# Performance work log

Measured on AMD Instinct MI355X. Metric: run time of the kernel, lower is better.

## Reference

```python
import jax, jax.numpy as jnp
import numpy as np

B, L, SH, EH, A, T = 128, 200, 512, 512, 512, 3


def setup_inputs() -> dict:
    key = jax.random.key(0)
    ks = jax.random.split(key, 13)
    s = 0.05  # small init scale to keep tanh/sigmoid unsaturated
    return {
        "sent_enc_doc": jax.random.normal(ks[0], (B, L, 2 * SH), jnp.float32),
        "h0_w": jax.random.normal(ks[1], (EH, SH), jnp.float32) * s,
        "h0_b": jax.random.normal(ks[2], (EH,), jnp.float32) * s,
        "gru_w_ih": jax.random.normal(ks[3], (3 * EH, 2 * SH), jnp.float32) * s,
        "gru_w_hh": jax.random.normal(ks[4], (3 * EH, EH), jnp.float32) * s,
        "gru_b_ih": jax.random.normal(ks[5], (3 * EH,), jnp.float32) * s,
        "gru_b_hh": jax.random.normal(ks[6], (3 * EH,), jnp.float32) * s,
        "wq": jax.random.normal(ks[7], (A, EH), jnp.float32) * s,
        "bq": jax.random.normal(ks[8], (A,), jnp.float32) * s,
        "wd": jax.random.normal(ks[9], (A, 2 * SH), jnp.float32) * s,
        "bd": jax.random.normal(ks[10], (A,), jnp.float32) * s,
        "ws": jax.random.normal(ks[11], (1, A), jnp.float32) * s,
        "bs": jax.random.normal(ks[12], (1,), jnp.float32) * s,
    }


def reference(sent_enc_doc, h0_w, h0_b, gru_w_ih, gru_w_hh, gru_b_ih, gru_b_hh,
              wq, bq, wd, bd, ws, bs):
    b, l, d2 = sent_enc_doc.shape
    sh = d2 // 2
    eh = gru_w_hh.shape[1]
    neg = jnp.asarray(-1e6, sent_enc_doc.dtype)

    # h0 = tanh(W * last backward vector), replicated across doc_len
    last_back = sent_enc_doc[:, 0, sh:]                      # (B, SH)
    h0 = jnp.tanh(last_back @ h0_w.T + h0_b)                 # (B, EH)
    h = jnp.broadcast_to(h0[:, None, :], (b, l, eh))         # (B, L, EH)

    s_prev = jnp.zeros((b, l, d2), sent_enc_doc.dtype)
    d_proj = sent_enc_doc @ wd.T + bd                        # (B, L, A) - loop-invariant
    mask = jnp.zeros((b, l), bool)
    rows = jnp.arange(b)

    scores_list, sel_list = [], []
    for _ in range(T):  # fixed, tiny, sequentially-dependent loop
        # GRUCell (torch gate order: r, z, n)
        gx = s_prev @ gru_w_ih.T + gru_b_ih                  # (B, L, 3EH)
        gh = h @ gru_w_hh.T + gru_b_hh                       # (B, L, 3EH)
        xr, xz, xn = jnp.split(gx, 3, axis=-1)
        hr, hz, hn = jnp.split(gh, 3, axis=-1)
        r = jax.nn.sigmoid(xr + hr)
        z = jax.nn.sigmoid(xz + hz)
        n = jnp.tanh(xn + r * hn)
        h = (1.0 - z) * n + z * h                            # (B, L, EH)

        # scorer: ws . tanh(Wq h + Wd s_i)
        score = (jnp.tanh(h @ wq.T + bq + d_proj) @ ws.T + bs)[..., 0]  # (B, L)
        score = jnp.where(mask, neg, score)
        idx = jnp.argmax(score, axis=1)                      # (B,)
        mask = mask.at[rows, idx].set(True)

        # gather the selected sentence encoding, broadcast to all positions
        s_sel = jnp.take_along_axis(sent_enc_doc, idx[:, None, None], axis=1)  # (B,1,2SH)
        s_prev = jnp.broadcast_to(s_sel, (b, l, d2))

        scores_list.append(score)
        sel_list.append(idx)

    sents_scores = jnp.stack(scores_list, axis=1)            # (B, T, L)
    sents_selected = jnp.stack(sel_list, axis=1)             # (B, T)
    return sents_scores, sents_selected
```

## Files before the change

kernel.cpp:

```cpp
#include <hip/hip_runtime.h>
#include <hip/hip_bf16.h>

constexpr int Bn  = 128;
constexpr int Ln  = 200;
constexpr int D2n = 1024;
constexpr int G3n = 1536;
constexpr int Tn  = 3;
constexpr int Nn  = 512;
constexpr int Kn  = 1024;

typedef unsigned short ushort;
typedef float f32x4 __attribute__((ext_vector_type(4)));
typedef __bf16 bf16x8 __attribute__((ext_vector_type(8)));

__device__ __forceinline__ ushort f2bf(float f) {
  unsigned u = __float_as_uint(f);
  unsigned r = (u + 0x7fffu + ((u >> 16) & 1u)) >> 16;
  return (ushort)r;
}
__device__ __forceinline__ float bf2f(ushort h) {
  return __uint_as_float(((unsigned)h) << 16);
}

__device__ __forceinline__ void gld_lds16(const ushort* g, ushort* l) {
  __builtin_amdgcn_global_load_lds(
      (const __attribute__((address_space(1))) unsigned int*)g,
      (__attribute__((address_space(3))) unsigned int*)l, 16, 0, 0);
}

__global__ void k_gather_lastb(const float* __restrict__ sent, float* __restrict__ lastb) {
  int i = blockIdx.x * 256 + threadIdx.x;
  int b = i >> 9, k = i & 511;
  lastb[i] = sent[(size_t)b * (Ln * D2n) + 512 + k];
}

__global__ void k_split(const float* __restrict__ W, ushort* __restrict__ hi,
                        ushort* __restrict__ lo) {
  int i = blockIdx.x * 256 + threadIdx.x;
  float4 v = ((const float4*)W)[i];
  ushort4 h, l;
  h.x = f2bf(v.x); l.x = f2bf(v.x - bf2f(h.x));
  h.y = f2bf(v.y); l.y = f2bf(v.y - bf2f(h.y));
  h.z = f2bf(v.z); l.z = f2bf(v.z - bf2f(h.z));
  h.w = f2bf(v.w); l.w = f2bf(v.w - bf2f(h.w));
  ((ushort4*)hi)[i] = h;
  ((ushort4*)lo)[i] = l;
}

template<int K, int ACT>
__launch_bounds__(256)
__global__ void k_small_gemm(const float* __restrict__ in, const float* __restrict__ W,
                             const float* __restrict__ bias, float* __restrict__ out, int J) {
  __shared__ float s[16 * K];
  const int b0 = blockIdx.y * 16;
  const int jl = threadIdx.x & 63;
  const int j  = blockIdx.x * 64 + jl;
  const int bg = (threadIdx.x >> 6) * 4;

  const float4* inp4 = (const float4*)(in + (size_t)b0 * K);
  float4* s4 = (float4*)s;
  for (int i = threadIdx.x; i < 4 * K; i += 256) s4[i] = inp4[i];
  __syncthreads();

  const float4* w4 = (const float4*)(W + (size_t)j * K);
  const float4* r0 = (const float4*)(s + (size_t)(bg + 0) * K);
  const float4* r1 = (const float4*)(s + (size_t)(bg + 1) * K);
  const float4* r2 = (const float4*)(s + (size_t)(bg + 2) * K);
  const float4* r3 = (const float4*)(s + (size_t)(bg + 3) * K);

  float acc0 = 0.f, acc1 = 0.f, acc2 = 0.f, acc3 = 0.f;
  #pragma unroll 4
  for (int k4 = 0; k4 < K / 4; ++k4) {
    float4 wv = w4[k4];
    float4 a;
    a = r0[k4]; acc0 += wv.x*a.x + wv.y*a.y + wv.z*a.z + wv.w*a.w;
    a = r1[k4]; acc1 += wv.x*a.x + wv.y*a.y + wv.z*a.z + wv.w*a.w;
    a = r2[k4]; acc2 += wv.x*a.x + wv.y*a.y + wv.z*a.z + wv.w*a.w;
    a = r3[k4]; acc3 += wv.x*a.x + wv.y*a.y + wv.z*a.z + wv.w*a.w;
  }
  float bb = bias[j];
  float v;
  v = acc0 + bb; if (ACT) v = tanhf(v); out[(size_t)(b0 + bg + 0) * J + j] = v;
  v = acc1 + bb; if (ACT) v = tanhf(v); out[(size_t)(b0 + bg + 1) * J + j] = v;
  v = acc2 + bb; if (ACT) v = tanhf(v); out[(size_t)(b0 + bg + 2) * J + j] = v;
  v = acc3 + bb; if (ACT) v = tanhf(v); out[(size_t)(b0 + bg + 3) * J + j] = v;
}

constexpr int NSTEP = Kn / 32;

__launch_bounds__(256)
__global__ void k_dproj_mfma(const ushort* __restrict__ Ahi, const ushort* __restrict__ Alo,
                             const ushort* __restrict__ Whi, const ushort* __restrict__ Wlo,
                             const float* __restrict__ bias, float* __restrict__ C) {
  __shared__ __align__(16) ushort sAh[128 * 32];
  __shared__ __align__(16) ushort sAl[128 * 32];
  __shared__ __align__(16) ushort sBh[128 * 32];
  __shared__ __align__(16) ushort sBl[128 * 32];

  const int bid = blockIdx.x;
  const int m0  = (bid % 200) * 128;
  const int n0  = (bid / 200) * 128;

  const int tid  = threadIdx.x;
  const int wave = tid >> 6, lane = tid & 63;
  const int wy = (wave >> 1) * 64, wx = (wave & 1) * 64;
  const int lm = lane & 15, lq = lane >> 4;

  const int fs = (lq ^ ((lm >> 1) & 3)) * 8;

  const int S0 = (wave * 2 + 0) * 64 + lane;
  const int S1 = (wave * 2 + 1) * 64 + lane;
  const int r0 = S0 >> 2, r1 = S1 >> 2;
  const int c0 = ((S0 & 3) ^ ((r0 >> 1) & 3)) * 8;
  const int c1 = ((S1 & 3) ^ ((r1 >> 1) & 3)) * 8;
  const ushort* pAh0 = Ahi + (size_t)(m0 + r0) * Kn + c0;
  const ushort* pAh1 = Ahi + (size_t)(m0 + r1) * Kn + c1;
  const ushort* pAl0 = Alo + (size_t)(m0 + r0) * Kn + c0;
  const ushort* pAl1 = Alo + (size_t)(m0 + r1) * Kn + c1;
  const ushort* pBh0 = Whi + (size_t)(n0 + r0) * Kn + c0;
  const ushort* pBh1 = Whi + (size_t)(n0 + r1) * Kn + c1;
  const ushort* pBl0 = Wlo + (size_t)(n0 + r0) * Kn + c0;
  const ushort* pBl1 = Wlo + (size_t)(n0 + r1) * Kn + c1;
  ushort* dA0 = &sAh[S0 * 8]; ushort* dA1 = &sAh[S1 * 8];
  ushort* dL0 = &sAl[S0 * 8]; ushort* dL1 = &sAl[S1 * 8];
  ushort* dB0 = &sBh[S0 * 8]; ushort* dB1 = &sBh[S1 * 8];
  ushort* dC0 = &sBl[S0 * 8]; ushort* dC1 = &sBl[S1 * 8];

  f32x4 acc[4][4] = {};

  for (int ks = 0; ks < NSTEP; ++ks) {
    const int ko = ks * 32;
    gld_lds16(pAh0 + ko, dA0); gld_lds16(pAh1 + ko, dA1);
    gld_lds16(pAl0 + ko, dL0); gld_lds16(pAl1 + ko, dL1);
    gld_lds16(pBh0 + ko, dB0); gld_lds16(pBh1 + ko, dB1);
    gld_lds16(pBl0 + ko, dC0); gld_lds16(pBl1 + ko, dC1);
    __syncthreads();

    bf16x8 ah[4], al[4], bh[4], bl[4];
    #pragma unroll
    for (int mi = 0; mi < 4; ++mi) {
      const int o = (wy + mi * 16 + lm) * 32 + fs;
      ah[mi] = *(const bf16x8*)&sAh[o];
      al[mi] = *(const bf16x8*)&sAl[o];
    }
    #pragma unroll
    for (int ni = 0; ni < 4; ++ni) {
      const int o = (wx + ni * 16 + lm) * 32 + fs;
      bh[ni] = *(const bf16x8*)&sBh[o];
      bl[ni] = *(const bf16x8*)&sBl[o];
    }
    #pragma unroll
    for (int mi = 0; mi < 4; ++mi)
      #pragma unroll
      for (int ni = 0; ni < 4; ++ni) {
        acc[mi][ni] = __builtin_amdgcn_mfma_f32_16x16x32_bf16(ah[mi], bh[ni], acc[mi][ni], 0, 0, 0);
        acc[mi][ni] = __builtin_amdgcn_mfma_f32_16x16x32_bf16(ah[mi], bl[ni], acc[mi][ni], 0, 0, 0);
        acc[mi][ni] = __builtin_amdgcn_mfma_f32_16x16x32_bf16(al[mi], bh[ni], acc[mi][ni], 0, 0, 0);
      }
    __syncthreads();
  }

  #pragma unroll
  for (int ni = 0; ni < 4; ++ni) {
    int col = n0 + wx + ni * 16 + lm;
    float bb = bias[col];
    #pragma unroll
    for (int mi = 0; mi < 4; ++mi) {
      int rbase = m0 + wy + mi * 16 + lq * 4;
      #pragma unroll
      for (int r = 0; r < 4; ++r)
        C[(size_t)(rbase + r) * Nn + col] = acc[mi][ni][r] + bb;
    }
  }
}

__global__ void k_gru_pw(const float* __restrict__ gx, const float* __restrict__ gh,
                         float* __restrict__ h) {
  int i = blockIdx.x * 256 + threadIdx.x;
  int b = i >> 9, j = i & 511;
  const float* gxb = gx + (size_t)b * G3n;
  const float* ghb = gh + (size_t)b * G3n;
  float rg = 1.f / (1.f + expf(-(gxb[j] + ghb[j])));
  float zg = 1.f / (1.f + expf(-(gxb[512 + j] + ghb[512 + j])));
  float ng = tanhf(gxb[1024 + j] + rg * ghb[1024 + j]);
  h[i] = (1.f - zg) * ng + zg * h[i];
}

__launch_bounds__(256)
__global__ void k_score(const float* __restrict__ dproj, const float* __restrict__ q,
                        const float* __restrict__ wsv, const float* __restrict__ bsv,
                        const int* __restrict__ mask, float* __restrict__ scoresf,
                        float* __restrict__ outScores, int t) {
  int w = blockIdx.x * 4 + (threadIdx.x >> 6);
  int lane = threadIdx.x & 63;
  int b = w / Ln, l = w % Ln;
  const float4* dp4 = (const float4*)(dproj + (size_t)w * Nn);
  const float4* q4  = (const float4*)(q + (size_t)b * Nn);
  const float4* ws4 = (const float4*)wsv;

  float sum = 0.f;
  #pragma unroll
  for (int i = 0; i < 2; ++i) {
    int idx = lane + i * 64;
    float4 d = dp4[idx], qq = q4[idx], wv = ws4[idx];
    sum += tanhf(qq.x + d.x) * wv.x + tanhf(qq.y + d.y) * wv.y
         + tanhf(qq.z + d.z) * wv.z + tanhf(qq.w + d.w) * wv.w;
  }
  #pragma unroll
  for (int off = 32; off > 0; off >>= 1) sum += __shfl_xor(sum, off, 64);

  if (lane == 0) {
    float v = sum + bsv[0];
    if (mask[w]) v = -1000000.0f;
    scoresf[w] = v;
    outScores[(size_t)b * (Tn * Ln) + t * Ln + l] = v;
  }
}

__launch_bounds__(256)
__global__ void k_argmax(const float* __restrict__ scoresf, const float* __restrict__ sent,
                         float* __restrict__ s_row, int* __restrict__ mask,
                         float* __restrict__ outSel, int t) {
  int b = blockIdx.x;
  __shared__ int s_idx;
  int tid = threadIdx.x;
  if (tid < 64) {
    const float* sc = scoresf + (size_t)b * Ln;
    float best = -3.0e38f; int bi = 0;
    for (int l = tid; l < Ln; l += 64) {
      float v = sc[l];
      if (v > best) { best = v; bi = l; }
    }
    #pragma unroll
    for (int off = 32; off > 0; off >>= 1) {
      float ov = __shfl_down(best, off, 64);
      int   oi = __shfl_down(bi,   off, 64);
      if (ov > best || (ov == best && oi < bi)) { best = ov; bi = oi; }
    }
    if (tid == 0) s_idx = bi;
  }
  __syncthreads();
  int idx = s_idx;
  const float* src = sent + ((size_t)b * Ln + idx) * D2n;
  float* dstp = s_row + (size_t)b * D2n;
  int k = tid * 4;
  *(float4*)(dstp + k) = *(const float4*)(src + k);
  if (tid == 0) {
    mask[b * Ln + idx] = 1;
    outSel[(size_t)b * Tn + t] = (float)idx;
  }
}

extern "C" void kernel_launch(void* const* d_in, const int* in_sizes, int n_in,
                              void* d_out, int out_size, void* d_ws, size_t ws_size,
                              hipStream_t stream) {
  const float* sent = (const float*)d_in[0];
  const float* h0_w = (const float*)d_in[1];
  const float* h0_b = (const float*)d_in[2];
  const float* w_ih = (const float*)d_in[3];
  const float* w_hh = (const float*)d_in[4];
  const float* b_ih = (const float*)d_in[5];
  const float* b_hh = (const float*)d_in[6];
  const float* wq   = (const float*)d_in[7];
  const float* bq   = (const float*)d_in[8];
  const float* wd   = (const float*)d_in[9];
  const float* bd   = (const float*)d_in[10];
  const float* wsv  = (const float*)d_in[11];
  const float* bsv  = (const float*)d_in[12];

  float* wsf     = (float*)d_ws;
  float* d_proj  = wsf;
  float* s_row   = d_proj + 13107200;
  float* h       = s_row + 131072;
  float* gx      = h + 65536;
  float* gh      = gx + 196608;
  float* lastb   = gh + 196608;
  float* q       = lastb + 65536;
  float* scoresf = q + 65536;
  int*   mask    = (int*)(scoresf + 25600);
  ushort* Whi    = (ushort*)(mask + 25600);
  ushort* Wlo    = Whi + 524288;
  ushort* Ahi    = Wlo + 524288;
  ushort* Alo    = Ahi + 26214400;

  float* outScores = (float*)d_out;
  float* outSel    = outScores + (size_t)Bn * Tn * Ln;

  hipMemsetAsync(s_row, 0, 131072 * sizeof(float), stream);
  hipMemsetAsync(mask, 0, 25600 * sizeof(int), stream);

  k_gather_lastb<<<256, 256, 0, stream>>>(sent, lastb);
  k_small_gemm<512, 1><<<dim3(8, 8), 256, 0, stream>>>(lastb, h0_w, h0_b, h, 512);
  k_split<<<512, 256, 0, stream>>>(wd, Whi, Wlo);
  k_split<<<25600, 256, 0, stream>>>(sent, Ahi, Alo);
  k_dproj_mfma<<<800, 256, 0, stream>>>(Ahi, Alo, Whi, Wlo, bd, d_proj);

  for (int t = 0; t < Tn; ++t) {
    k_small_gemm<1024, 0><<<dim3(24, 8), 256, 0, stream>>>(s_row, w_ih, b_ih, gx, G3n);
    k_small_gemm<512, 0><<<dim3(24, 8), 256, 0, stream>>>(h, w_hh, b_hh, gh, G3n);
    k_gru_pw<<<256, 256, 0, stream>>>(gx, gh, h);
    k_small_gemm<512, 0><<<dim3(8, 8), 256, 0, stream>>>(h, wq, bq, q, 512);
    k_score<<<6400, 256, 0, stream>>>(d_proj, q, wsv, bsv, mask, scoresf, outScores, t);
    k_argmax<<<128, 256, 0, stream>>>(scoresf, sent, s_row, mask, outSel, t);
  }
}
```

Measured before the change: 619.3 us.

## Fuse GRU gate GEMMs with pointwise update, transpose weights, atomic-packed argmax

The two gate GEMMs and the GRU pointwise kernel are replaced by one fused kernel that reads pre-transposed W_ih/W_hh with coalesced column access and splits K across two wave halves. The query projection likewise uses a transposed Wq. Argmax now happens inside the score kernel through a 64-bit atomicMax on a packed (ordered float, inverted index) key, so the argmax kernel only decodes the key. This removes per-step launches and intermediate gx/gh traffic, at the cost of three transposes per call and per-row atomic contention.

```diff
diff --git a/kernel.cpp b/kernel.cpp
--- a/kernel.cpp
+++ b/kernel.cpp
@@ -26,6 +26,12 @@
   __builtin_amdgcn_global_load_lds(
       (const __attribute__((address_space(1))) unsigned int*)g,
       (__attribute__((address_space(3))) unsigned int*)l, 16, 0, 0);
+}
+
+__device__ __forceinline__ unsigned long long score_key(float v, int l) {
+  unsigned u = __float_as_uint(v);
+  unsigned k32 = (u & 0x80000000u) ? ~u : (u | 0x80000000u);
+  return ((unsigned long long)k32 << 32) | (unsigned)(~l);
 }
 
 __global__ void k_gather_lastb(const float* __restrict__ sent, float* __restrict__ lastb) {
@@ -45,6 +51,20 @@
   h.w = f2bf(v.w); l.w = f2bf(v.w - bf2f(h.w));
   ((ushort4*)hi)[i] = h;
   ((ushort4*)lo)[i] = l;
+}
+
+__global__ void k_transp(const float* __restrict__ in, float* __restrict__ out,
+                         int R, int C) {
+  __shared__ float t[32][33];
+  const int x = threadIdx.x, y = threadIdx.y;
+  const int c0 = blockIdx.x * 32, r0 = blockIdx.y * 32;
+  #pragma unroll
+  for (int i = 0; i < 4; ++i)
+    t[y + i * 8][x] = in[(size_t)(r0 + y + i * 8) * C + c0 + x];
+  __syncthreads();
+  #pragma unroll
+  for (int i = 0; i < 4; ++i)
+    out[(size_t)(c0 + y + i * 8) * R + r0 + x] = t[x][y + i * 8];
 }
 
 template<int K, int ACT>
@@ -174,22 +194,110 @@
   }
 }
 
-__global__ void k_gru_pw(const float* __restrict__ gx, const float* __restrict__ gh,
-                         float* __restrict__ h) {
-  int i = blockIdx.x * 256 + threadIdx.x;
-  int b = i >> 9, j = i & 511;
-  const float* gxb = gx + (size_t)b * G3n;
-  const float* ghb = gh + (size_t)b * G3n;
-  float rg = 1.f / (1.f + expf(-(gxb[j] + ghb[j])));
-  float zg = 1.f / (1.f + expf(-(gxb[512 + j] + ghb[512 + j])));
-  float ng = tanhf(gxb[1024 + j] + rg * ghb[1024 + j]);
-  h[i] = (1.f - zg) * ng + zg * h[i];
+__launch_bounds__(512)
+__global__ void k_gru(const float* __restrict__ s_row, const float* __restrict__ h_old,
+                      const float* __restrict__ wihT, const float* __restrict__ whhT,
+                      const float* __restrict__ b_ih, const float* __restrict__ b_hh,
+                      float* __restrict__ h_new) {
+  __shared__ __align__(16) float sS[4][1024];
+  __shared__ __align__(16) float sH[4][512];
+  __shared__ float sP[256][6];
+
+  const int tid  = threadIdx.x;
+  const int lane = tid & 63;
+  const int wave = tid >> 6;
+  const int b_loc = wave & 3, kh = wave >> 2;
+  const int jt = blockIdx.x & 7, bt = blockIdx.x >> 3;
+  const int j  = jt * 64 + lane;
+
+  {
+    const float4* src = (const float4*)(s_row + (size_t)bt * 4 * 1024);
+    float4* dst = (float4*)&sS[0][0];
+    dst[tid] = src[tid];
+    dst[tid + 512] = src[tid + 512];
+    ((float4*)&sH[0][0])[tid] = ((const float4*)(h_old + (size_t)bt * 4 * 512))[tid];
+  }
+  __syncthreads();
+
+  float xr = 0, xz = 0, xn = 0, hr = 0, hz = 0, hn = 0;
+  {
+    const float* w = wihT + (size_t)(kh * 512) * G3n + j;
+    const float4* sv4 = (const float4*)&sS[b_loc][kh * 512];
+    #pragma unroll 2
+    for (int k4 = 0; k4 < 128; ++k4) {
+      float4 sv = sv4[k4];
+      xr += w[0] * sv.x; xz += w[512] * sv.x; xn += w[1024] * sv.x; w += G3n;
+      xr += w[0] * sv.y; xz += w[512] * sv.y; xn += w[1024] * sv.y; w += G3n;
+      xr += w[0] * sv.z; xz += w[512] * sv.z; xn += w[1024] * sv.z; w += G3n;
+      xr += w[0] * sv.w; xz += w[512] * sv.w; xn += w[1024] * sv.w; w += G3n;
+    }
+  }
+  {
+    const float* w = whhT + (size_t)(kh * 256) * G3n + j;
+    const float4* hv4 = (const float4*)&sH[b_loc][kh * 256];
+    #pragma unroll 2
+    for (int k4 = 0; k4 < 64; ++k4) {
+      float4 hv = hv4[k4];
+      hr += w[0] * hv.x; hz += w[512] * hv.x; hn += w[1024] * hv.x; w += G3n;
+      hr += w[0] * hv.y; hz += w[512] * hv.y; hn += w[1024] * hv.y; w += G3n;
+      hr += w[0] * hv.z; hz += w[512] * hv.z; hn += w[1024] * hv.z; w += G3n;
+      hr += w[0] * hv.w; hz += w[512] * hv.w; hn += w[1024] * hv.w; w += G3n;
+    }
+  }
+  const int pidx = b_loc * 64 + lane;
+  if (kh) {
+    sP[pidx][0] = xr; sP[pidx][1] = xz; sP[pidx][2] = xn;
+    sP[pidx][3] = hr; sP[pidx][4] = hz; sP[pidx][5] = hn;
+  }
+  __syncthreads();
+  if (!kh) {
+    xr += sP[pidx][0]; xz += sP[pidx][1]; xn += sP[pidx][2];
+    hr += sP[pidx][3]; hz += sP[pidx][4]; hn += sP[pidx][5];
+    xr += b_ih[j];        hr += b_hh[j];
+    xz += b_ih[512 + j];  hz += b_hh[512 + j];
+    xn += b_ih[1024 + j]; hn += b_hh[1024 + j];
+    float r = 1.f / (1.f + expf(-(xr + hr)));
+    float z = 1.f / (1.f + expf(-(xz + hz)));
+    float n = tanhf(xn + r * hn);
+    const int b = bt * 4 + b_loc;
+    float hold = sH[b_loc][j];
+    h_new[(size_t)b * 512 + j] = (1.f - z) * n + z * hold;
+  }
+}
+
+__launch_bounds__(256)
+__global__ void k_qT(const float* __restrict__ h, const float* __restrict__ wqT,
+                     const float* __restrict__ bq, float* __restrict__ q) {
+  __shared__ __align__(16) float sH[4][512];
+  const int tid = threadIdx.x, lane = tid & 63, bw = tid >> 6;
+  const int jt = blockIdx.x & 7, bt = blockIdx.x >> 3;
+  const int j = jt * 64 + lane;
+  {
+    float4* dst = (float4*)&sH[0][0];
+    const float4* src = (const float4*)(h + (size_t)bt * 2048);
+    dst[tid] = src[tid];
+    dst[tid + 256] = src[tid + 256];
+  }
+  __syncthreads();
+  float acc = 0.f;
+  const float* w = wqT + j;
+  const float4* hv4 = (const float4*)&sH[bw][0];
+  #pragma unroll 4
+  for (int k4 = 0; k4 < 128; ++k4) {
+    float4 hv = hv4[k4];
+    acc += w[0] * hv.x; w += 512;
+    acc += w[0] * hv.y; w += 512;
+    acc += w[0] * hv.z; w += 512;
+    acc += w[0] * hv.w; w += 512;
+  }
+  const int b = bt * 4 + bw;
+  q[(size_t)b * 512 + j] = acc + bq[j];
 }
 
 __launch_bounds__(256)
 __global__ void k_score(const float* __restrict__ dproj, const float* __restrict__ q,
                         const float* __restrict__ wsv, const float* __restrict__ bsv,
-                        const int* __restrict__ mask, float* __restrict__ scoresf,
+                        const int* __restrict__ mask, unsigned long long* __restrict__ packed,
                         float* __restrict__ outScores, int t) {
   int w = blockIdx.x * 4 + (threadIdx.x >> 6);
   int lane = threadIdx.x & 63;
@@ -212,32 +320,22 @@
   if (lane == 0) {
     float v = sum + bsv[0];
     if (mask[w]) v = -1000000.0f;
-    scoresf[w] = v;
     outScores[(size_t)b * (Tn * Ln) + t * Ln + l] = v;
+    atomicMax(&packed[b], score_key(v, l));
   }
 }
 
 __launch_bounds__(256)
-__global__ void k_argmax(const float* __restrict__ scoresf, const float* __restrict__ sent,
+__global__ void k_argmax(unsigned long long* __restrict__ packed,
+                         const float* __restrict__ sent,
                          float* __restrict__ s_row, int* __restrict__ mask,
                          float* __restrict__ outSel, int t) {
   int b = blockIdx.x;
   __shared__ int s_idx;
   int tid = threadIdx.x;
-  if (tid < 64) {
-    const float* sc = scoresf + (size_t)b * Ln;
-    float best = -3.0e38f; int bi = 0;
-    for (int l = tid; l < Ln; l += 64) {
-      float v = sc[l];
-      if (v > best) { best = v; bi = l; }
-    }
-    #pragma unroll
-    for (int off = 32; off > 0; off >>= 1) {
-      float ov = __shfl_down(best, off, 64);
-      int   oi = __shfl_down(bi,   off, 64);
-      if (ov > best || (ov == best && oi < bi)) { best = ov; bi = oi; }
-    }
-    if (tid == 0) s_idx = bi;
+  if (tid == 0) {
+    unsigned long long key = packed[b];
+    s_idx = (int)(~(unsigned)(key & 0xFFFFFFFFull));
   }
   __syncthreads();
   int idx = s_idx;
@@ -248,6 +346,7 @@
   if (tid == 0) {
     mask[b * Ln + idx] = 1;
     outSel[(size_t)b * Tn + t] = (float)idx;
+    packed[b] = 0ull;
   }
 }
 
@@ -271,14 +370,16 @@
   float* wsf     = (float*)d_ws;
   float* d_proj  = wsf;
   float* s_row   = d_proj + 13107200;
-  float* h       = s_row + 131072;
-  float* gx      = h + 65536;
-  float* gh      = gx + 196608;
-  float* lastb   = gh + 196608;
+  float* hA      = s_row + 131072;
+  float* hB      = hA + 65536;
+  float* lastb   = hB + 65536;
   float* q       = lastb + 65536;
-  float* scoresf = q + 65536;
-  int*   mask    = (int*)(scoresf + 25600);
-  ushort* Whi    = (ushort*)(mask + 25600);
+  float* wihT    = q + 65536;
+  float* whhT    = wihT + 1572864;
+  float* wqT     = whhT + 786432;
+  int*   mask    = (int*)(wqT + 262144);
+  unsigned long long* packed = (unsigned long long*)(mask + 25600);
+  ushort* Whi    = (ushort*)(packed + 128);
   ushort* Wlo    = Whi + 524288;
   ushort* Ahi    = Wlo + 524288;
   ushort* Alo    = Ahi + 26214400;
@@ -288,19 +389,24 @@
 
   hipMemsetAsync(s_row, 0, 131072 * sizeof(float), stream);
   hipMemsetAsync(mask, 0, 25600 * sizeof(int), stream);
+  hipMemsetAsync(packed, 0, 128 * sizeof(unsigned long long), stream);
 
   k_gather_lastb<<<256, 256, 0, stream>>>(sent, lastb);
-  k_small_gemm<512, 1><<<dim3(8, 8), 256, 0, stream>>>(lastb, h0_w, h0_b, h, 512);
+  k_small_gemm<512, 1><<<dim3(8, 8), 256, 0, stream>>>(lastb, h0_w, h0_b, hA, 512);
+  k_transp<<<dim3(32, 48), dim3(32, 8), 0, stream>>>(w_ih, wihT, 1536, 1024);
+  k_transp<<<dim3(16, 48), dim3(32, 8), 0, stream>>>(w_hh, whhT, 1536, 512);
+  k_transp<<<dim3(16, 16), dim3(32, 8), 0, stream>>>(wq, wqT, 512, 512);
   k_split<<<512, 256, 0, stream>>>(wd, Whi, Wlo);
   k_split<<<25600, 256, 0, stream>>>(sent, Ahi, Alo);
   k_dproj_mfma<<<800, 256, 0, stream>>>(Ahi, Alo, Whi, Wlo, bd, d_proj);
 
+  float* hc = hA;
+  float* hn = hB;
   for (int t = 0; t < Tn; ++t) {
-    k_small_gemm<1024, 0><<<dim3(24, 8), 256, 0, stream>>>(s_row, w_ih, b_ih, gx, G3n);
-    k_small_gemm<512, 0><<<dim3(24, 8), 256, 0, stream>>>(h, w_hh, b_hh, gh, G3n);
-    k_gru_pw<<<256, 256, 0, stream>>>(gx, gh, h);
-    k_small_gemm<512, 0><<<dim3(8, 8), 256, 0, stream>>>(h, wq, bq, q, 512);
-    k_score<<<6400, 256, 0, stream>>>(d_proj, q, wsv, bsv, mask, scoresf, outScores, t);
-    k_argmax<<<128, 256, 0, stream>>>(scoresf, sent, s_row, mask, outSel, t);
-  }
-}
+    k_gru<<<256, 512, 0, stream>>>(s_row, hc, wihT, whhT, b_ih, b_hh, hn);
+    k_qT<<<256, 256, 0, stream>>>(hn, wqT, bq, q);
+    k_score<<<6400, 256, 0, stream>>>(d_proj, q, wsv, bsv, mask, packed, outScores, t);
+    k_argmax<<<128, 256, 0, stream>>>(packed, sent, s_row, mask, outSel, t);
+    float* tmp = hc; hc = hn; hn = tmp;
+  }
+}
```

Result: slower. 752.9 us (+21.6%).

## Fuse the per-step GRU/score/argmax loop into one cooperative persistent kernel

Applied to the files above, without the earlier changes.

Replaces the 18 per-timestep kernel launches with a single cooperative kernel of 256 blocks that loops over the three steps and separates stages with grid-wide syncs. The gx and gh GEMMs now run in the same phase instead of two launches. This removes launch overhead and inter-kernel gaps. The cost is grid.sync overhead, lower parallelism for the score stage (256 blocks looping over 6400 work items), and a 64KB shared buffer per block that limits occupancy.

```diff
diff --git a/kernel.cpp b/kernel.cpp
--- a/kernel.cpp
+++ b/kernel.cpp
@@ -1,5 +1,8 @@
 #include <hip/hip_runtime.h>
 #include <hip/hip_bf16.h>
+#include <hip/hip_cooperative_groups.h>
+
+namespace cg = cooperative_groups;
 
 constexpr int Bn  = 128;
 constexpr int Ln  = 200;
@@ -48,18 +51,20 @@
 }
 
 template<int K, int ACT>
-__launch_bounds__(256)
-__global__ void k_small_gemm(const float* __restrict__ in, const float* __restrict__ W,
-                             const float* __restrict__ bias, float* __restrict__ out, int J) {
-  __shared__ float s[16 * K];
-  const int b0 = blockIdx.y * 16;
-  const int jl = threadIdx.x & 63;
-  const int j  = blockIdx.x * 64 + jl;
-  const int bg = (threadIdx.x >> 6) * 4;
+__device__ __forceinline__ void gemm_work(const float* __restrict__ in,
+                                          const float* __restrict__ W,
+                                          const float* __restrict__ bias,
+                                          float* __restrict__ out, int J,
+                                          int jt, int bt, float* s) {
+  const int tid = threadIdx.x;
+  const int b0 = bt * 16;
+  const int jl = tid & 63;
+  const int j  = jt * 64 + jl;
+  const int bg = (tid >> 6) * 4;
 
   const float4* inp4 = (const float4*)(in + (size_t)b0 * K);
   float4* s4 = (float4*)s;
-  for (int i = threadIdx.x; i < 4 * K; i += 256) s4[i] = inp4[i];
+  for (int i = tid; i < 4 * K; i += 256) s4[i] = inp4[i];
   __syncthreads();
 
   const float4* w4 = (const float4*)(W + (size_t)j * K);
@@ -84,6 +89,15 @@
   v = acc1 + bb; if (ACT) v = tanhf(v); out[(size_t)(b0 + bg + 1) * J + j] = v;
   v = acc2 + bb; if (ACT) v = tanhf(v); out[(size_t)(b0 + bg + 2) * J + j] = v;
   v = acc3 + bb; if (ACT) v = tanhf(v); out[(size_t)(b0 + bg + 3) * J + j] = v;
+  __syncthreads();
+}
+
+template<int K, int ACT>
+__launch_bounds__(256)
+__global__ void k_small_gemm(const float* __restrict__ in, const float* __restrict__ W,
+                             const float* __restrict__ bias, float* __restrict__ out, int J) {
+  __shared__ float s[16 * K];
+  gemm_work<K, ACT>(in, W, bias, out, J, blockIdx.x, blockIdx.y, s);
 }
 
 constexpr int NSTEP = Kn / 32;
@@ -174,80 +188,105 @@
   }
 }
 
-__global__ void k_gru_pw(const float* __restrict__ gx, const float* __restrict__ gh,
-                         float* __restrict__ h) {
-  int i = blockIdx.x * 256 + threadIdx.x;
-  int b = i >> 9, j = i & 511;
-  const float* gxb = gx + (size_t)b * G3n;
-  const float* ghb = gh + (size_t)b * G3n;
-  float rg = 1.f / (1.f + expf(-(gxb[j] + ghb[j])));
-  float zg = 1.f / (1.f + expf(-(gxb[512 + j] + ghb[512 + j])));
-  float ng = tanhf(gxb[1024 + j] + rg * ghb[1024 + j]);
-  h[i] = (1.f - zg) * ng + zg * h[i];
-}
-
 __launch_bounds__(256)
-__global__ void k_score(const float* __restrict__ dproj, const float* __restrict__ q,
+__global__ void k_tloop(const float* __restrict__ sent,
+                        const float* __restrict__ w_ih, const float* __restrict__ w_hh,
+                        const float* __restrict__ b_ih, const float* __restrict__ b_hh,
+                        const float* __restrict__ wq, const float* __restrict__ bq,
                         const float* __restrict__ wsv, const float* __restrict__ bsv,
-                        const int* __restrict__ mask, float* __restrict__ scoresf,
-                        float* __restrict__ outScores, int t) {
-  int w = blockIdx.x * 4 + (threadIdx.x >> 6);
-  int lane = threadIdx.x & 63;
-  int b = w / Ln, l = w % Ln;
-  const float4* dp4 = (const float4*)(dproj + (size_t)w * Nn);
-  const float4* q4  = (const float4*)(q + (size_t)b * Nn);
-  const float4* ws4 = (const float4*)wsv;
-
-  float sum = 0.f;
-  #pragma unroll
-  for (int i = 0; i < 2; ++i) {
-    int idx = lane + i * 64;
-    float4 d = dp4[idx], qq = q4[idx], wv = ws4[idx];
-    sum += tanhf(qq.x + d.x) * wv.x + tanhf(qq.y + d.y) * wv.y
-         + tanhf(qq.z + d.z) * wv.z + tanhf(qq.w + d.w) * wv.w;
-  }
-  #pragma unroll
-  for (int off = 32; off > 0; off >>= 1) sum += __shfl_xor(sum, off, 64);
-
-  if (lane == 0) {
-    float v = sum + bsv[0];
-    if (mask[w]) v = -1000000.0f;
-    scoresf[w] = v;
-    outScores[(size_t)b * (Tn * Ln) + t * Ln + l] = v;
-  }
-}
-
-__launch_bounds__(256)
-__global__ void k_argmax(const float* __restrict__ scoresf, const float* __restrict__ sent,
-                         float* __restrict__ s_row, int* __restrict__ mask,
-                         float* __restrict__ outSel, int t) {
-  int b = blockIdx.x;
+                        const float* __restrict__ dproj,
+                        float* __restrict__ s_row, float* __restrict__ h,
+                        float* __restrict__ gx, float* __restrict__ gh,
+                        float* __restrict__ q, float* __restrict__ scoresf,
+                        int* __restrict__ mask,
+                        float* __restrict__ outScores, float* __restrict__ outSel) {
+  cg::grid_group grid = cg::this_grid();
+  __shared__ float sbuf[16 * 1024];
   __shared__ int s_idx;
-  int tid = threadIdx.x;
-  if (tid < 64) {
-    const float* sc = scoresf + (size_t)b * Ln;
-    float best = -3.0e38f; int bi = 0;
-    for (int l = tid; l < Ln; l += 64) {
-      float v = sc[l];
-      if (v > best) { best = v; bi = l; }
-    }
-    #pragma unroll
-    for (int off = 32; off > 0; off >>= 1) {
-      float ov = __shfl_down(best, off, 64);
-      int   oi = __shfl_down(bi,   off, 64);
-      if (ov > best || (ov == best && oi < bi)) { best = ov; bi = oi; }
-    }
-    if (tid == 0) s_idx = bi;
-  }
-  __syncthreads();
-  int idx = s_idx;
-  const float* src = sent + ((size_t)b * Ln + idx) * D2n;
-  float* dstp = s_row + (size_t)b * D2n;
-  int k = tid * 4;
-  *(float4*)(dstp + k) = *(const float4*)(src + k);
-  if (tid == 0) {
-    mask[b * Ln + idx] = 1;
-    outSel[(size_t)b * Tn + t] = (float)idx;
+
+  const int bid = blockIdx.x;
+  const int tid = threadIdx.x;
+
+  for (int t = 0; t < Tn; ++t) {
+    for (int w = bid; w < 384; w += 256) {
+      if (w < 192) gemm_work<1024, 0>(s_row, w_ih, b_ih, gx, G3n, w % 24, w / 24, sbuf);
+      else { int v = w - 192; gemm_work<512, 0>(h, w_hh, b_hh, gh, G3n, v % 24, v / 24, sbuf); }
+    }
+    grid.sync();
+
+    {
+      int i = bid * 256 + tid;
+      int b = i >> 9, j = i & 511;
+      const float* gxb = gx + (size_t)b * G3n;
+      const float* ghb = gh + (size_t)b * G3n;
+      float rg = 1.f / (1.f + expf(-(gxb[j] + ghb[j])));
+      float zg = 1.f / (1.f + expf(-(gxb[512 + j] + ghb[512 + j])));
+      float ng = tanhf(gxb[1024 + j] + rg * ghb[1024 + j]);
+      h[i] = (1.f - zg) * ng + zg * h[i];
+    }
+    grid.sync();
+
+    for (int w = bid; w < 64; w += 256)
+      gemm_work<512, 0>(h, wq, bq, q, 512, w % 8, w / 8, sbuf);
+    grid.sync();
+
+    for (int blk = bid; blk < 6400; blk += 256) {
+      int w = blk * 4 + (tid >> 6);
+      int lane = tid & 63;
+      int b = w / Ln, l = w % Ln;
+      const float4* dp4 = (const float4*)(dproj + (size_t)w * Nn);
+      const float4* q4  = (const float4*)(q + (size_t)b * Nn);
+      const float4* ws4 = (const float4*)wsv;
+
+      float sum = 0.f;
+      #pragma unroll
+      for (int i = 0; i < 2; ++i) {
+        int idx = lane + i * 64;
+        float4 d = dp4[idx], qq = q4[idx], wv = ws4[idx];
+        sum += tanhf(qq.x + d.x) * wv.x + tanhf(qq.y + d.y) * wv.y
+             + tanhf(qq.z + d.z) * wv.z + tanhf(qq.w + d.w) * wv.w;
+      }
+      #pragma unroll
+      for (int off = 32; off > 0; off >>= 1) sum += __shfl_xor(sum, off, 64);
+
+      if (lane == 0) {
+        float v = sum + bsv[0];
+        if (mask[w]) v = -1000000.0f;
+        scoresf[w] = v;
+        outScores[(size_t)b * (Tn * Ln) + t * Ln + l] = v;
+      }
+    }
+    grid.sync();
+
+    for (int b = bid; b < 128; b += 256) {
+      if (tid < 64) {
+        const float* sc = scoresf + (size_t)b * Ln;
+        float best = -3.0e38f; int bi = 0;
+        for (int l = tid; l < Ln; l += 64) {
+          float v = sc[l];
+          if (v > best) { best = v; bi = l; }
+        }
+        #pragma unroll
+        for (int off = 32; off > 0; off >>= 1) {
+          float ov = __shfl_down(best, off, 64);
+          int   oi = __shfl_down(bi,   off, 64);
+          if (ov > best || (ov == best && oi < bi)) { best = ov; bi = oi; }
+        }
+        if (tid == 0) s_idx = bi;
+      }
+      __syncthreads();
+      int idx = s_idx;
+      const float* src = sent + ((size_t)b * Ln + idx) * D2n;
+      float* dstp = s_row + (size_t)b * D2n;
+      int k = tid * 4;
+      *(float4*)(dstp + k) = *(const float4*)(src + k);
+      if (tid == 0) {
+        mask[b * Ln + idx] = 1;
+        outSel[(size_t)b * Tn + t] = (float)idx;
+      }
+      __syncthreads();
+    }
+    grid.sync();
   }
 }
 
@@ -295,12 +334,11 @@
   k_split<<<25600, 256, 0, stream>>>(sent, Ahi, Alo);
   k_dproj_mfma<<<800, 256, 0, stream>>>(Ahi, Alo, Whi, Wlo, bd, d_proj);
 
-  for (int t = 0; t < Tn; ++t) {
-    k_small_gemm<1024, 0><<<dim3(24, 8), 256, 0, stream>>>(s_row, w_ih, b_ih, gx, G3n);
-    k_small_gemm<512, 0><<<dim3(24, 8), 256, 0, stream>>>(h, w_hh, b_hh, gh, G3n);
-    k_gru_pw<<<256, 256, 0, stream>>>(gx, gh, h);
-    k_small_gemm<512, 0><<<dim3(8, 8), 256, 0, stream>>>(h, wq, bq, q, 512);
-    k_score<<<6400, 256, 0, stream>>>(d_proj, q, wsv, bsv, mask, scoresf, outScores, t);
-    k_argmax<<<128, 256, 0, stream>>>(scoresf, sent, s_row, mask, outSel, t);
-  }
-}
+  void* args[] = {
+    (void*)&sent, (void*)&w_ih, (void*)&w_hh, (void*)&b_ih, (void*)&b_hh,
+    (void*)&wq, (void*)&bq, (void*)&wsv, (void*)&bsv, (void*)&d_proj,
+    (void*)&s_row, (void*)&h, (void*)&gx, (void*)&gh, (void*)&q,
+    (void*)&scoresf, (void*)&mask, (void*)&outScores, (void*)&outSel
+  };
+  hipLaunchCooperativeKernel((void*)k_tloop, dim3(256), dim3(256), args, 0, stream);
+}
```

New measurement: 1.100 ms. 1.78x slower.

## Move GRU gate and query GEMMs to split-bf16 MFMA with fused gate epilogue

Applied to the files above, without the earlier changes.

Replaces the scalar fp32 small GEMMs for gx, gh and q with MFMA kernels that use hi/lo bf16 splits of the weights and activations. A new k_gates kernel computes the input and hidden gate products and applies the GRU pointwise update in its epilogue. It writes h and its bf16 split directly, and h is double-buffered across steps. The aim is to cut launches and intermediate gx/gh traffic and to use matrix cores. The cost is per-call weight split kernels and a gate kernel that runs only 16 blocks, so it has low parallelism.

```diff
diff --git a/kernel.cpp b/kernel.cpp
--- a/kernel.cpp
+++ b/kernel.cpp
@@ -86,26 +86,21 @@
   v = acc3 + bb; if (ACT) v = tanhf(v); out[(size_t)(b0 + bg + 3) * J + j] = v;
 }
 
-constexpr int NSTEP = Kn / 32;
-
-__launch_bounds__(256)
-__global__ void k_dproj_mfma(const ushort* __restrict__ Ahi, const ushort* __restrict__ Alo,
-                             const ushort* __restrict__ Whi, const ushort* __restrict__ Wlo,
-                             const float* __restrict__ bias, float* __restrict__ C) {
+template<int KK>
+__device__ __forceinline__ void mfma_tile128(
+    const ushort* __restrict__ Ah, const ushort* __restrict__ Al,
+    const ushort* __restrict__ Bh, const ushort* __restrict__ Bl,
+    const float* __restrict__ bias, float* __restrict__ C, int ldc,
+    int m0, int n0) {
   __shared__ __align__(16) ushort sAh[128 * 32];
   __shared__ __align__(16) ushort sAl[128 * 32];
   __shared__ __align__(16) ushort sBh[128 * 32];
   __shared__ __align__(16) ushort sBl[128 * 32];
 
-  const int bid = blockIdx.x;
-  const int m0  = (bid % 200) * 128;
-  const int n0  = (bid / 200) * 128;
-
   const int tid  = threadIdx.x;
   const int wave = tid >> 6, lane = tid & 63;
   const int wy = (wave >> 1) * 64, wx = (wave & 1) * 64;
   const int lm = lane & 15, lq = lane >> 4;
-
   const int fs = (lq ^ ((lm >> 1) & 3)) * 8;
 
   const int S0 = (wave * 2 + 0) * 64 + lane;
@@ -113,14 +108,14 @@
   const int r0 = S0 >> 2, r1 = S1 >> 2;
   const int c0 = ((S0 & 3) ^ ((r0 >> 1) & 3)) * 8;
   const int c1 = ((S1 & 3) ^ ((r1 >> 1) & 3)) * 8;
-  const ushort* pAh0 = Ahi + (size_t)(m0 + r0) * Kn + c0;
-  const ushort* pAh1 = Ahi + (size_t)(m0 + r1) * Kn + c1;
-  const ushort* pAl0 = Alo + (size_t)(m0 + r0) * Kn + c0;
-  const ushort* pAl1 = Alo + (size_t)(m0 + r1) * Kn + c1;
-  const ushort* pBh0 = Whi + (size_t)(n0 + r0) * Kn + c0;
-  const ushort* pBh1 = Whi + (size_t)(n0 + r1) * Kn + c1;
-  const ushort* pBl0 = Wlo + (size_t)(n0 + r0) * Kn + c0;
-  const ushort* pBl1 = Wlo + (size_t)(n0 + r1) * Kn + c1;
+  const ushort* pAh0 = Ah + (size_t)(m0 + r0) * KK + c0;
+  const ushort* pAh1 = Ah + (size_t)(m0 + r1) * KK + c1;
+  const ushort* pAl0 = Al + (size_t)(m0 + r0) * KK + c0;
+  const ushort* pAl1 = Al + (size_t)(m0 + r1) * KK + c1;
+  const ushort* pBh0 = Bh + (size_t)(n0 + r0) * KK + c0;
+  const ushort* pBh1 = Bh + (size_t)(n0 + r1) * KK + c1;
+  const ushort* pBl0 = Bl + (size_t)(n0 + r0) * KK + c0;
+  const ushort* pBl1 = Bl + (size_t)(n0 + r1) * KK + c1;
   ushort* dA0 = &sAh[S0 * 8]; ushort* dA1 = &sAh[S1 * 8];
   ushort* dL0 = &sAl[S0 * 8]; ushort* dL1 = &sAl[S1 * 8];
   ushort* dB0 = &sBh[S0 * 8]; ushort* dB1 = &sBh[S1 * 8];
@@ -128,7 +123,7 @@
 
   f32x4 acc[4][4] = {};
 
-  for (int ks = 0; ks < NSTEP; ++ks) {
+  for (int ks = 0; ks < KK / 32; ++ks) {
     const int ko = ks * 32;
     gld_lds16(pAh0 + ko, dA0); gld_lds16(pAh1 + ko, dA1);
     gld_lds16(pAl0 + ko, dL0); gld_lds16(pAl1 + ko, dL1);
@@ -169,21 +164,160 @@
       int rbase = m0 + wy + mi * 16 + lq * 4;
       #pragma unroll
       for (int r = 0; r < 4; ++r)
-        C[(size_t)(rbase + r) * Nn + col] = acc[mi][ni][r] + bb;
-    }
-  }
-}
-
-__global__ void k_gru_pw(const float* __restrict__ gx, const float* __restrict__ gh,
-                         float* __restrict__ h) {
-  int i = blockIdx.x * 256 + threadIdx.x;
-  int b = i >> 9, j = i & 511;
-  const float* gxb = gx + (size_t)b * G3n;
-  const float* ghb = gh + (size_t)b * G3n;
-  float rg = 1.f / (1.f + expf(-(gxb[j] + ghb[j])));
-  float zg = 1.f / (1.f + expf(-(gxb[512 + j] + ghb[512 + j])));
-  float ng = tanhf(gxb[1024 + j] + rg * ghb[1024 + j]);
-  h[i] = (1.f - zg) * ng + zg * h[i];
+        C[(size_t)(rbase + r) * ldc + col] = acc[mi][ni][r] + bb;
+    }
+  }
+}
+
+__launch_bounds__(256)
+__global__ void k_dproj_mfma(const ushort* __restrict__ Ahi, const ushort* __restrict__ Alo,
+                             const ushort* __restrict__ Whi, const ushort* __restrict__ Wlo,
+                             const float* __restrict__ bias, float* __restrict__ C) {
+  const int bid = blockIdx.x;
+  mfma_tile128<1024>(Ahi, Alo, Whi, Wlo, bias, C, Nn, (bid % 200) * 128, (bid / 200) * 128);
+}
+
+__launch_bounds__(256)
+__global__ void k_q_mfma(const ushort* __restrict__ hh, const ushort* __restrict__ hl,
+                         const ushort* __restrict__ WqH, const ushort* __restrict__ WqL,
+                         const float* __restrict__ bq, float* __restrict__ q) {
+  mfma_tile128<512>(hh, hl, WqH, WqL, bq, q, 512, 0, blockIdx.x * 128);
+}
+
+__launch_bounds__(256)
+__global__ void k_gates(const ushort* __restrict__ sxh, const ushort* __restrict__ sxl,
+                        const float* __restrict__ hOld,
+                        const ushort* __restrict__ hh, const ushort* __restrict__ hl,
+                        const ushort* __restrict__ WihH, const ushort* __restrict__ WihL,
+                        const ushort* __restrict__ WhhH, const ushort* __restrict__ WhhL,
+                        const float* __restrict__ b_ih, const float* __restrict__ b_hh,
+                        float* __restrict__ hNew, ushort* __restrict__ hhN,
+                        ushort* __restrict__ hlN) {
+  __shared__ __align__(16) ushort sAh[128 * 32];
+  __shared__ __align__(16) ushort sAl[128 * 32];
+  __shared__ __align__(16) ushort sWh[96 * 32];
+  __shared__ __align__(16) ushort sWl[96 * 32];
+
+  const int j0 = blockIdx.x * 32;
+  const int tid = threadIdx.x, wave = tid >> 6, lane = tid & 63;
+  const int wy = wave * 32;
+  const int lm = lane & 15, lq = lane >> 4;
+  const int fs = (lq ^ ((lm >> 1) & 3)) * 8;
+
+  const int rA0 = tid >> 2;
+  const int cA0 = ((tid & 3) ^ ((rA0 >> 1) & 3)) * 8;
+  const int SA1 = tid + 256;
+  const int rA1 = SA1 >> 2;
+  const int cA1 = ((SA1 & 3) ^ ((rA1 >> 1) & 3)) * 8;
+  const int gw0 = (rA0 >> 5) * 512 + j0 + (rA0 & 31);
+  const int gw1 = (rA1 >> 5) * 512 + j0 + (rA1 & 31);
+  const bool w1on = tid < 128;
+
+  f32x4 ax[3][2][2] = {};
+  f32x4 ag[3][2][2] = {};
+
+  for (int ks = 0; ks < 32; ++ks) {
+    const int ko = ks * 32;
+    gld_lds16(sxh + (size_t)rA0 * 1024 + ko + cA0, &sAh[tid * 8]);
+    gld_lds16(sxh + (size_t)rA1 * 1024 + ko + cA1, &sAh[SA1 * 8]);
+    gld_lds16(sxl + (size_t)rA0 * 1024 + ko + cA0, &sAl[tid * 8]);
+    gld_lds16(sxl + (size_t)rA1 * 1024 + ko + cA1, &sAl[SA1 * 8]);
+    gld_lds16(WihH + (size_t)gw0 * 1024 + ko + cA0, &sWh[tid * 8]);
+    gld_lds16(WihL + (size_t)gw0 * 1024 + ko + cA0, &sWl[tid * 8]);
+    if (w1on) {
+      gld_lds16(WihH + (size_t)gw1 * 1024 + ko + cA1, &sWh[SA1 * 8]);
+      gld_lds16(WihL + (size_t)gw1 * 1024 + ko + cA1, &sWl[SA1 * 8]);
+    }
+    __syncthreads();
+
+    bf16x8 fah[2], fal[2];
+    #pragma unroll
+    for (int mi = 0; mi < 2; ++mi) {
+      const int o = (wy + mi * 16 + lm) * 32 + fs;
+      fah[mi] = *(const bf16x8*)&sAh[o];
+      fal[mi] = *(const bf16x8*)&sAl[o];
+    }
+    #pragma unroll
+    for (int g = 0; g < 3; ++g)
+      #pragma unroll
+      for (int ni = 0; ni < 2; ++ni) {
+        const int o = (g * 32 + ni * 16 + lm) * 32 + fs;
+        bf16x8 fbh = *(const bf16x8*)&sWh[o];
+        bf16x8 fbl = *(const bf16x8*)&sWl[o];
+        #pragma unroll
+        for (int mi = 0; mi < 2; ++mi) {
+          ax[g][mi][ni] = __builtin_amdgcn_mfma_f32_16x16x32_bf16(fah[mi], fbh, ax[g][mi][ni], 0, 0, 0);
+          ax[g][mi][ni] = __builtin_amdgcn_mfma_f32_16x16x32_bf16(fah[mi], fbl, ax[g][mi][ni], 0, 0, 0);
+          ax[g][mi][ni] = __builtin_amdgcn_mfma_f32_16x16x32_bf16(fal[mi], fbh, ax[g][mi][ni], 0, 0, 0);
+        }
+      }
+    __syncthreads();
+  }
+
+  for (int ks = 0; ks < 16; ++ks) {
+    const int ko = ks * 32;
+    gld_lds16(hh + (size_t)rA0 * 512 + ko + cA0, &sAh[tid * 8]);
+    gld_lds16(hh + (size_t)rA1 * 512 + ko + cA1, &sAh[SA1 * 8]);
+    gld_lds16(hl + (size_t)rA0 * 512 + ko + cA0, &sAl[tid * 8]);
+    gld_lds16(hl + (size_t)rA1 * 512 + ko + cA1, &sAl[SA1 * 8]);
+    gld_lds16(WhhH + (size_t)gw0 * 512 + ko + cA0, &sWh[tid * 8]);
+    gld_lds16(WhhL + (size_t)gw0 * 512 + ko + cA0, &sWl[tid * 8]);
+    if (w1on) {
+      gld_lds16(WhhH + (size_t)gw1 * 512 + ko + cA1, &sWh[SA1 * 8]);
+      gld_lds16(WhhL + (size_t)gw1 * 512 + ko + cA1, &sWl[SA1 * 8]);
+    }
+    __syncthreads();
+
+    bf16x8 fah[2], fal[2];
+    #pragma unroll
+    for (int mi = 0; mi < 2; ++mi) {
+      const int o = (wy + mi * 16 + lm) * 32 + fs;
+      fah[mi] = *(const bf16x8*)&sAh[o];
+      fal[mi] = *(const bf16x8*)&sAl[o];
+    }
+    #pragma unroll
+    for (int g = 0; g < 3; ++g)
+      #pragma unroll
+      for (int ni = 0; ni < 2; ++ni) {
+        const int o = (g * 32 + ni * 16 + lm) * 32 + fs;
+        bf16x8 fbh = *(const bf16x8*)&sWh[o];
+        bf16x8 fbl = *(const bf16x8*)&sWl[o];
+        #pragma unroll
+        for (int mi = 0; mi < 2; ++mi) {
+          ag[g][mi][ni] = __builtin_amdgcn_mfma_f32_16x16x32_bf16(fah[mi], fbh, ag[g][mi][ni], 0, 0, 0);
+          ag[g][mi][ni] = __builtin_amdgcn_mfma_f32_16x16x32_bf16(fah[mi], fbl, ag[g][mi][ni], 0, 0, 0);
+          ag[g][mi][ni] = __builtin_amdgcn_mfma_f32_16x16x32_bf16(fal[mi], fbh, ag[g][mi][ni], 0, 0, 0);
+        }
+      }
+    __syncthreads();
+  }
+
+  #pragma unroll
+  for (int ni = 0; ni < 2; ++ni) {
+    const int j = j0 + ni * 16 + lm;
+    const float bir = b_ih[j], biz = b_ih[512 + j], bin = b_ih[1024 + j];
+    const float bhr = b_hh[j], bhz = b_hh[512 + j], bhn = b_hh[1024 + j];
+    #pragma unroll
+    for (int mi = 0; mi < 2; ++mi) {
+      const int rbase = wy + mi * 16 + lq * 4;
+      #pragma unroll
+      for (int rr = 0; rr < 4; ++rr) {
+        const int b = rbase + rr;
+        float xr = ax[0][mi][ni][rr] + bir, hr = ag[0][mi][ni][rr] + bhr;
+        float xz = ax[1][mi][ni][rr] + biz, hz = ag[1][mi][ni][rr] + bhz;
+        float xn = ax[2][mi][ni][rr] + bin, hn = ag[2][mi][ni][rr] + bhn;
+        float r = 1.f / (1.f + expf(-(xr + hr)));
+        float z = 1.f / (1.f + expf(-(xz + hz)));
+        float n = tanhf(xn + r * hn);
+        float hv = hOld[(size_t)b * 512 + j];
+        float hw = (1.f - z) * n + z * hv;
+        hNew[(size_t)b * 512 + j] = hw;
+        ushort hbf = f2bf(hw);
+        hhN[(size_t)b * 512 + j] = hbf;
+        hlN[(size_t)b * 512 + j] = f2bf(hw - bf2f(hbf));
+      }
+    }
+  }
 }
 
 __launch_bounds__(256)
@@ -218,9 +352,10 @@
 }
 
 __launch_bounds__(256)
-__global__ void k_argmax(const float* __restrict__ scoresf, const float* __restrict__ sent,
-                         float* __restrict__ s_row, int* __restrict__ mask,
-                         float* __restrict__ outSel, int t) {
+__global__ void k_argmax(const float* __restrict__ scoresf,
+                         const float* __restrict__ sent,
+                         ushort* __restrict__ s_rowh, ushort* __restrict__ s_rowl,
+                         int* __restrict__ mask, float* __restrict__ outSel, int t) {
   int b = blockIdx.x;
   __shared__ int s_idx;
   int tid = threadIdx.x;
@@ -242,9 +377,15 @@
   __syncthreads();
   int idx = s_idx;
   const float* src = sent + ((size_t)b * Ln + idx) * D2n;
-  float* dstp = s_row + (size_t)b * D2n;
   int k = tid * 4;
-  *(float4*)(dstp + k) = *(const float4*)(src + k);
+  float4 v = *(const float4*)(src + k);
+  ushort4 hvec, lvec;
+  hvec.x = f2bf(v.x); lvec.x = f2bf(v.x - bf2f(hvec.x));
+  hvec.y = f2bf(v.y); lvec.y = f2bf(v.y - bf2f(hvec.y));
+  hvec.z = f2bf(v.z); lvec.z = f2bf(v.z - bf2f(hvec.z));
+  hvec.w = f2bf(v.w); lvec.w = f2bf(v.w - bf2f(hvec.w));
+  *(ushort4*)(s_rowh + (size_t)b * 1024 + k) = hvec;
+  *(ushort4*)(s_rowl + (size_t)b * 1024 + k) = lvec;
   if (tid == 0) {
     mask[b * Ln + idx] = 1;
     outSel[(size_t)b * Tn + t] = (float)idx;
@@ -270,11 +411,9 @@
 
   float* wsf     = (float*)d_ws;
   float* d_proj  = wsf;
-  float* s_row   = d_proj + 13107200;
-  float* h       = s_row + 131072;
-  float* gx      = h + 65536;
-  float* gh      = gx + 196608;
-  float* lastb   = gh + 196608;
+  float* hA      = d_proj + 13107200;
+  float* hB      = hA + 65536;
+  float* lastb   = hB + 65536;
   float* q       = lastb + 65536;
   float* scoresf = q + 65536;
   int*   mask    = (int*)(scoresf + 25600);
@@ -283,24 +422,47 @@
   ushort* Ahi    = Wlo + 524288;
   ushort* Alo    = Ahi + 26214400;
 
+  ushort* WihH   = Ahi;
+  ushort* WihL   = WihH + 1572864;
+  ushort* WhhH   = WihL + 1572864;
+  ushort* WhhL   = WhhH + 786432;
+  ushort* WqH    = WhhL + 786432;
+  ushort* WqL    = WqH + 262144;
+  ushort* hhA    = WqL + 262144;
+  ushort* hlA    = hhA + 65536;
+  ushort* hhB    = hlA + 65536;
+  ushort* hlB    = hhB + 65536;
+  ushort* s_rowh = hlB + 65536;
+  ushort* s_rowl = s_rowh + 131072;
+
   float* outScores = (float*)d_out;
   float* outSel    = outScores + (size_t)Bn * Tn * Ln;
 
-  hipMemsetAsync(s_row, 0, 131072 * sizeof(float), stream);
   hipMemsetAsync(mask, 0, 25600 * sizeof(int), stream);
 
   k_gather_lastb<<<256, 256, 0, stream>>>(sent, lastb);
-  k_small_gemm<512, 1><<<dim3(8, 8), 256, 0, stream>>>(lastb, h0_w, h0_b, h, 512);
-  k_split<<<512, 256, 0, stream>>>(wd, Whi, Wlo);
+  k_small_gemm<512, 1><<<dim3(8, 8), 256, 0, stream>>>(lastb, h0_w, h0_b, hA, 512);
+  k_split<<<512,   256, 0, stream>>>(wd, Whi, Wlo);
   k_split<<<25600, 256, 0, stream>>>(sent, Ahi, Alo);
   k_dproj_mfma<<<800, 256, 0, stream>>>(Ahi, Alo, Whi, Wlo, bd, d_proj);
 
+  hipMemsetAsync(s_rowh, 0, 2 * 131072 * sizeof(ushort), stream);
+  k_split<<<1536,  256, 0, stream>>>(w_ih, WihH, WihL);
+  k_split<<<768,   256, 0, stream>>>(w_hh, WhhH, WhhL);
+  k_split<<<256,   256, 0, stream>>>(wq, WqH, WqL);
+  k_split<<<64,    256, 0, stream>>>(hA, hhA, hlA);
+
+  float* hc = hA;  ushort* hhc = hhA; ushort* hlc = hlA;
+  float* hn = hB;  ushort* hhn = hhB; ushort* hln = hlB;
   for (int t = 0; t < Tn; ++t) {
-    k_small_gemm<1024, 0><<<dim3(24, 8), 256, 0, stream>>>(s_row, w_ih, b_ih, gx, G3n);
-    k_small_gemm<512, 0><<<dim3(24, 8), 256, 0, stream>>>(h, w_hh, b_hh, gh, G3n);
-    k_gru_pw<<<256, 256, 0, stream>>>(gx, gh, h);
-    k_small_gemm<512, 0><<<dim3(8, 8), 256, 0, stream>>>(h, wq, bq, q, 512);
+    k_gates<<<16, 256, 0, stream>>>(s_rowh, s_rowl, hc, hhc, hlc,
+                                    WihH, WihL, WhhH, WhhL, b_ih, b_hh,
+                                    hn, hhn, hln);
+    k_q_mfma<<<4, 256, 0, stream>>>(hhn, hln, WqH, WqL, bq, q);
     k_score<<<6400, 256, 0, stream>>>(d_proj, q, wsv, bsv, mask, scoresf, outScores, t);
-    k_argmax<<<128, 256, 0, stream>>>(scoresf, sent, s_row, mask, outSel, t);
-  }
-}
+    k_argmax<<<128, 256, 0, stream>>>(scoresf, sent, s_rowh, s_rowl, mask, outSel, t);
+    float* tf = hc; hc = hn; hn = tf;
+    ushort* t1 = hhc; hhc = hhn; hhn = t1;
+    ushort* t2 = hlc; hlc = hln; hln = t2;
+  }
+}
```

New measurement: 592.6 us. -4.3%, faster.
